# Kernel tuning notes

Measured on AMD Instinct MI355X. Metric: run time of the kernel, lower is better.

Reference implementation:

```python
import jax, jax.numpy as jnp
import numpy as np

N_NODES = 50000
N_EDGES = 800000
D_NODE = 128
D_EDGE = 64
N_GC = 2
H = 256
N_GRAPHS = 512


def setup_inputs() -> dict:
    key = jax.random.key(0)
    ks = jax.random.split(key, 32)
    s = 0.05
    inp = {
        'x': jax.random.normal(ks[0], (N_NODES, D_NODE), jnp.float32),
        'edge_index': jax.random.randint(ks[1], (2, N_EDGES), 0, N_NODES, jnp.int64 if jax.config.jax_enable_x64 else jnp.int32),
        'edge_attr': jax.random.normal(ks[2], (N_EDGES, D_EDGE), jnp.float32),
        'batch': jnp.sort(jax.random.randint(ks[3], (N_NODES,), 0, N_GRAPHS)),
    }
    zin = 2 * D_NODE + D_EDGE  # 320
    inp['conv_Wf'] = jax.random.normal(ks[4], (N_GC, D_NODE, zin), jnp.float32) * s
    inp['conv_bf'] = jnp.zeros((N_GC, D_NODE), jnp.float32)
    inp['conv_Ws'] = jax.random.normal(ks[5], (N_GC, D_NODE, zin), jnp.float32) * s
    inp['conv_bs'] = jnp.zeros((N_GC, D_NODE), jnp.float32)
    # mlp_1: Linear(128->256), ReLU, Linear(256->256), ReLU, proj Linear(256->128)
    inp['mlp1_W0'] = jax.random.normal(ks[6], (H, D_NODE), jnp.float32) * s
    inp['mlp1_b0'] = jnp.zeros((H,), jnp.float32)
    inp['mlp1_W1'] = jax.random.normal(ks[7], (H, H), jnp.float32) * s
    inp['mlp1_b1'] = jnp.zeros((H,), jnp.float32)
    inp['mlp1_Wp'] = jax.random.normal(ks[8], (D_NODE, H), jnp.float32) * s
    inp['mlp1_bp'] = jnp.zeros((D_NODE,), jnp.float32)
    # mlp_2: same structure
    inp['mlp2_W0'] = jax.random.normal(ks[9], (H, D_NODE), jnp.float32) * s
    inp['mlp2_b0'] = jnp.zeros((H,), jnp.float32)
    inp['mlp2_W1'] = jax.random.normal(ks[10], (H, H), jnp.float32) * s
    inp['mlp2_b1'] = jnp.zeros((H,), jnp.float32)
    inp['mlp2_Wp'] = jax.random.normal(ks[11], (D_NODE, H), jnp.float32) * s
    inp['mlp2_bp'] = jnp.zeros((D_NODE,), jnp.float32)
    inp['out_W'] = jax.random.normal(ks[12], (1, D_NODE), jnp.float32) * s
    inp['out_b'] = jnp.zeros((1,), jnp.float32)
    return inp


def _mlp(x, W0, b0, W1, b1, Wp, bp):
    h = jax.nn.relu(x @ W0.T + b0)
    h = jax.nn.relu(h @ W1.T + b1)
    return h @ Wp.T + bp


def _cgconv(x, src, dst, edge_attr, Wf, bf, Ws, bs):
    # z = [x_i (target), x_j (source), edge_attr]  -> [E, 2D+De]
    z = jnp.concatenate([x[dst], x[src], edge_attr], axis=-1)
    msg = jax.nn.sigmoid(z @ Wf.T + bf) * jax.nn.softplus(z @ Ws.T + bs)
    aggr = jax.ops.segment_sum(msg, dst, num_segments=x.shape[0])
    return x + aggr  # CGConv residual


def reference(x, edge_index, edge_attr, batch,
              conv_Wf, conv_bf, conv_Ws, conv_bs,
              mlp1_W0, mlp1_b0, mlp1_W1, mlp1_b1, mlp1_Wp, mlp1_bp,
              mlp2_W0, mlp2_b0, mlp2_W1, mlp2_b1, mlp2_Wp, mlp2_bp,
              out_W, out_b):
    src, dst = edge_index[0], edge_index[1]
    out = x
    for l in range(N_GC):
        out = _cgconv(out, src, dst, edge_attr, conv_Wf[l], conv_bf[l], conv_Ws[l], conv_bs[l])
    out = out + _mlp(out, mlp1_W0, mlp1_b0, mlp1_W1, mlp1_b1, mlp1_Wp, mlp1_bp)
    out = jax.ops.segment_sum(out, batch, num_segments=N_GRAPHS)  # global_add_pool
    out = out + _mlp(out, mlp2_W0, mlp2_b0, mlp2_W1, mlp2_b1, mlp2_Wp, mlp2_bp)
    out = out @ out_W.T + out_b  # [n_graphs, 1]
    return out
```

## Files before the change

### kernel.cpp

```cpp
#include <hip/hip_runtime.h>
#include <stdint.h>

#define NN 50000
#define NE 800000
#define DN 128
#define DE 64
#define NG 512
#define HD 256
#define LDA 72
#define SPK_S 132

typedef unsigned short ushort_t;
typedef __attribute__((ext_vector_type(8))) short short8;
typedef __attribute__((ext_vector_type(4))) float floatx4;

__device__ __forceinline__ float bf2f(ushort_t h){ unsigned u=((unsigned)h)<<16; float f; __builtin_memcpy(&f,&u,4); return f; }
__device__ __forceinline__ float bflo(unsigned u){ unsigned v=u<<16; float f; __builtin_memcpy(&f,&v,4); return f; }
__device__ __forceinline__ float bfhi(unsigned u){ unsigned v=u&0xffff0000u; float f; __builtin_memcpy(&f,&v,4); return f; }
__device__ __forceinline__ ushort_t f2bf(float f){ unsigned u; __builtin_memcpy(&u,&f,4); u += 0x7FFFu + ((u>>16)&1u); return (ushort_t)(u>>16); }
__device__ __forceinline__ unsigned pk2(float a,float b){ return (unsigned)f2bf(a) | ((unsigned)f2bf(b)<<16); }

__global__ void k_conv_node_w(const float* Wf, const float* Ws, ushort_t* out){
  int i = blockIdx.x*256 + threadIdx.x;
  if(i >= 2*512*128) return;
  int l = i >> 16;
  int r = i & 65535;
  int n = r >> 7, k = r & 127;
  const float* W = (n<256)? Wf : Ws;
  int nn = n & 127;
  int koff = ((n>>7)&1) ? 128+k : k;
  out[i] = f2bf(W[(size_t)l*128*320 + (size_t)nn*320 + koff]);
}

__global__ void k_conv_edge_w(const float* Wf, const float* Ws, ushort_t* out){
  int i = blockIdx.x*256 + threadIdx.x;
  if(i >= 2*256*64) return;
  int l = i >> 14;
  int r = i & 16383;
  int n = r >> 6, k = r & 63;
  const float* W = (n<128)? Wf : Ws;
  int nn = n & 127;
  out[i] = f2bf(W[(size_t)l*128*320 + (size_t)nn*320 + 256 + k]);
}

__global__ void k_f2bf(const float* s, ushort_t* d, int n){
  int i = blockIdx.x*256 + threadIdx.x;
  if(i<n) d[i] = f2bf(s[i]);
}

__global__ void k_init_x(const float* x, float* xcur, ushort_t* xb){
  int i = blockIdx.x*256 + threadIdx.x;
  if(i < NN*DN){ float v = x[i]; xcur[i]=v; xb[i]=f2bf(v); }
}

__global__ void k_zero_u32(unsigned* p, int n){
  int i = blockIdx.x*256 + threadIdx.x;
  if(i<n) p[i]=0u;
}

__global__ void k_hist(const int* dst, int* deg){
  int i = blockIdx.x*256 + threadIdx.x;
  if(i<NE) atomicAdd(&deg[dst[i]], 1);
}

__global__ void k_blocksum(const int* deg, int* bsum, int n){
  __shared__ int s[256];
  int t = threadIdx.x, i = blockIdx.x*256 + t;
  s[t] = (i<n)? deg[i] : 0;
  __syncthreads();
  for(int o=128;o>0;o>>=1){ if(t<o) s[t]+=s[t+o]; __syncthreads(); }
  if(t==0) bsum[blockIdx.x]=s[0];
}

__global__ void k_scan_bsum(int* bsum, int nb, int* offs, int nnodes){
  __shared__ int s[2][256];
  int t = threadIdx.x;
  int v = (t<nb)? bsum[t] : 0;
  s[0][t]=v; __syncthreads();
  int cur=0;
  for(int o=1;o<256;o<<=1){
    int nx=cur^1;
    s[nx][t] = s[cur][t] + ((t>=o)? s[cur][t-o] : 0);
    cur=nx; __syncthreads();
  }
  if(t<nb) bsum[t] = s[cur][t] - v;
  if(t==255) offs[nnodes] = s[cur][255];
}

__global__ void k_scanscatter(const int* deg, const int* bsum, int* offs, int* cursor, int n){
  __shared__ int s[2][256];
  int t=threadIdx.x, i=blockIdx.x*256+t;
  int v=(i<n)? deg[i] : 0;
  s[0][t]=v; __syncthreads();
  int cur=0;
  for(int o=1;o<256;o<<=1){
    int nx=cur^1;
    s[nx][t] = s[cur][t] + ((t>=o)? s[cur][t-o] : 0);
    cur=nx; __syncthreads();
  }
  if(i<n){ int ex = s[cur][t]-v + bsum[blockIdx.x]; offs[i]=ex; cursor[i]=ex; }
}

__global__ void k_scatter(const int* dst, int* cursor, int* eid){
  int i = blockIdx.x*256 + threadIdx.x;
  if(i<NE){ int pos = atomicAdd(&cursor[dst[i]], 1); eid[pos]=i; }
}

__global__ __launch_bounds__(256) void k_gemm(const ushort_t* __restrict__ Ain, const ushort_t* __restrict__ Wg,
      int M, int N, int K, const float* __restrict__ bias, int mode,
      ushort_t* __restrict__ outb, float* __restrict__ outf, const float* __restrict__ addf){
  __shared__ __align__(16) ushort_t As[64*LDA];
  __shared__ __align__(16) ushort_t Bs[64*LDA];
  int tid = threadIdx.x;
  int m0 = blockIdx.x*64, n0 = blockIdx.y*64;
  int w = tid>>6, lane = tid&63, row16 = lane&15, quad = lane>>4;
  floatx4 acc[4];
  #pragma unroll
  for(int t=0;t<4;t++) acc[t]=(floatx4)(0.f);
  int nk = K>>6;
  for(int kc=0; kc<nk; kc++){
    #pragma unroll
    for(int i=0;i<2;i++){
      int lin = tid + i*256;
      int row = lin>>3, c8 = (lin&7)*8;
      uint4 va;
      int gm = m0+row;
      if(gm < M) va = *(const uint4*)&Ain[(size_t)gm*K + kc*64 + c8];
      else va = make_uint4(0,0,0,0);
      *(uint4*)&As[row*LDA + c8] = va;
      uint4 vb = *(const uint4*)&Wg[(size_t)(n0+row)*K + kc*64 + c8];
      *(uint4*)&Bs[row*LDA + c8] = vb;
    }
    __syncthreads();
    #pragma unroll
    for(int ks=0;ks<2;ks++){
      short8 a = *(const short8*)&As[(w*16+row16)*LDA + ks*32 + quad*8];
      #pragma unroll
      for(int t=0;t<4;t++){
        short8 b = *(const short8*)&Bs[(t*16+row16)*LDA + ks*32 + quad*8];
        acc[t] = __builtin_amdgcn_mfma_f32_16x16x32_bf16(a,b,acc[t],0,0,0);
      }
    }
    __syncthreads();
  }
  #pragma unroll
  for(int t=0;t<4;t++){
    int nn = n0 + t*16 + row16;
    #pragma unroll
    for(int r=0;r<4;r++){
      int m = m0 + w*16 + quad*4 + r;
      if(m>=M) continue;
      float v = acc[t][r];
      if(mode==1){ v += bias[nn]; v = v>0.f? v:0.f; outb[(size_t)m*N+nn]=f2bf(v); }
      else if(mode==2){ v += bias[nn] + addf[(size_t)m*N+nn]; outf[(size_t)m*N+nn]=v; }
      else { outb[(size_t)m*N+nn]=f2bf(v); }
    }
  }
}

__global__ __launch_bounds__(256) void k_edge_msg(const float* __restrict__ ea,
      const int* __restrict__ src_g, const int* __restrict__ dst_g,
      const ushort_t* __restrict__ Wedge, const ushort_t* __restrict__ Atab,
      const float* __restrict__ bf, const float* __restrict__ bs,
      ushort_t* __restrict__ msg){
  __shared__ __align__(16) char smem[47616];
  ushort_t* We  = (ushort_t*)smem;
  unsigned* spk = (unsigned*)smem;
  ushort_t* el  = (ushort_t*)(smem + 36864);
  int*      dl  = (int*)(smem + 46080);
  int*      sl  = (int*)(smem + 46336);
  float*    bfl = (float*)(smem + 46592);
  float*    bsl = (float*)(smem + 47104);

  int tid = threadIdx.x;
  int e0 = blockIdx.x*64;
  {
    const uint4* s = (const uint4*)Wedge;
    #pragma unroll
    for(int i=0;i<8;i++){
      int idx = tid + i*256;
      int row = idx>>3, col = (idx&7)*8;
      *(uint4*)&We[row*LDA + col] = s[idx];
    }
  }
  {
    int row = tid>>2, c0 = (tid&3)*16;
    const float4* p = (const float4*)&ea[(size_t)(e0+row)*64 + c0];
    float4 f0=p[0], f1=p[1], f2=p[2], f3=p[3];
    uint4 q0, q1;
    q0.x=pk2(f0.x,f0.y); q0.y=pk2(f0.z,f0.w); q0.z=pk2(f1.x,f1.y); q0.w=pk2(f1.z,f1.w);
    q1.x=pk2(f2.x,f2.y); q1.y=pk2(f2.z,f2.w); q1.z=pk2(f3.x,f3.y); q1.w=pk2(f3.z,f3.w);
    *(uint4*)&el[row*LDA + c0] = q0;
    *(uint4*)&el[row*LDA + c0 + 8] = q1;
  }
  if(tid<64){ dl[tid]=dst_g[e0+tid]; sl[tid]=src_g[e0+tid]; }
  if(tid>=128 && tid<256){ int t2=tid-128; bfl[t2]=bf[t2]; }
  if(tid<128){ bsl[tid]=bs[tid]; }
  __syncthreads();

  int w = tid>>6, lane = tid&63, row16 = lane&15, quad = lane>>4;
  floatx4 acc[16];
  #pragma unroll
  for(int t=0;t<16;t++) acc[t]=(floatx4)(0.f);
  #pragma unroll
  for(int ks=0;ks<2;ks++){
    short8 a = *(const short8*)&el[(w*16+row16)*LDA + ks*32 + quad*8];
    #pragma unroll
    for(int t=0;t<16;t++){
      short8 b = *(const short8*)&We[(t*16+row16)*LDA + ks*32 + quad*8];
      acc[t]=__builtin_amdgcn_mfma_f32_16x16x32_bf16(a,b,acc[t],0,0,0);
    }
  }
  __syncthreads();

  #pragma unroll
  for(int t=0;t<8;t++){
    int c = t*16 + row16;
    float bfc = bfl[c], bsc = bsl[c];
    #pragma unroll
    for(int r=0;r<4;r++){
      int rl = w*16 + quad*4 + r;
      spk[rl*SPK_S + c] = pk2(acc[t][r] + bfc, acc[t+8][r] + bsc);
    }
  }
  __syncthreads();

  #pragma unroll
  for(int j=0;j<4;j++){
    int id  = j*256 + tid;
    int eli = id >> 4;
    int c0  = (id & 15) * 8;
    int d = dl[eli], s = sl[eli];
    const unsigned* base = &spk[eli*SPK_S + c0];
    uint4 q0 = *(const uint4*)(base);
    uint4 q1 = *(const uint4*)(base + 4);
    const ushort_t* Adp = Atab + (size_t)d*512;
    const ushort_t* Asp = Atab + (size_t)s*512;
    uint4 a0 = *(const uint4*)&Adp[c0];
    uint4 a1 = *(const uint4*)&Asp[128+c0];
    uint4 a2 = *(const uint4*)&Adp[256+c0];
    uint4 a3 = *(const uint4*)&Asp[384+c0];
    unsigned qs[8] = {q0.x,q0.y,q0.z,q0.w,q1.x,q1.y,q1.z,q1.w};
    unsigned A0[4] = {a0.x,a0.y,a0.z,a0.w};
    unsigned A1[4] = {a1.x,a1.y,a1.z,a1.w};
    unsigned A2[4] = {a2.x,a2.y,a2.z,a2.w};
    unsigned A3[4] = {a3.x,a3.y,a3.z,a3.w};
    unsigned outw[4];
    #pragma unroll
    for(int k=0;k<4;k++){
      float fv0 = bflo(qs[2*k])   + bflo(A0[k]) + bflo(A1[k]);
      float sv0 = bfhi(qs[2*k])   + bflo(A2[k]) + bflo(A3[k]);
      float fv1 = bflo(qs[2*k+1]) + bfhi(A0[k]) + bfhi(A1[k]);
      float sv1 = bfhi(qs[2*k+1]) + bfhi(A2[k]) + bfhi(A3[k]);
      float sig0 = 1.f/(1.f+__expf(-fv0));
      float sig1 = 1.f/(1.f+__expf(-fv1));
      float sp0  = fmaxf(sv0,0.f) + __logf(1.f+__expf(-fabsf(sv0)));
      float sp1  = fmaxf(sv1,0.f) + __logf(1.f+__expf(-fabsf(sv1)));
      outw[k] = pk2(sig0*sp0, sig1*sp1);
    }
    uint4 o4; o4.x=outw[0]; o4.y=outw[1]; o4.z=outw[2]; o4.w=outw[3];
    *(uint4*)&msg[(size_t)(e0+eli)*128 + c0] = o4;
  }
}

__global__ __launch_bounds__(256) void k_aggregate(const ushort_t* __restrict__ msg,
      const int* __restrict__ eid, const int* __restrict__ offs,
      float* __restrict__ xcur, ushort_t* __restrict__ xb){
  int v = blockIdx.x*4 + (threadIdx.x>>6);
  int lane = threadIdx.x & 63;
  int c0 = lane*2;
  float2 a = *(float2*)&xcur[(size_t)v*128 + c0];
  int b = offs[v], e_ = offs[v+1];
  for(int j=b;j<e_;j++){
    int e = eid[j];
    unsigned mm = *(const unsigned*)&msg[(size_t)e*128 + c0];
    a.x += bflo(mm);
    a.y += bfhi(mm);
  }
  *(float2*)&xcur[(size_t)v*128 + c0] = a;
  *(unsigned*)&xb[(size_t)v*128 + c0] = pk2(a.x, a.y);
}

__global__ __launch_bounds__(256) void k_pool(const float* __restrict__ xcur,
      const int* __restrict__ batch, float* __restrict__ pooled){
  int b0 = blockIdx.x * 128;
  int ch = threadIdx.x & 127;
  int half = threadIdx.x >> 7;
  int n0 = b0 + half*64;
  if(n0 >= NN) return;
  int n1 = n0 + 64; if(n1 > NN) n1 = NN;
  float sum = 0.f;
  int bid = batch[n0];
  for(int n=n0; n<n1; n++){
    int b = batch[n];
    if(b != bid){ atomicAdd(&pooled[(size_t)bid*128+ch], sum); sum=0.f; bid=b; }
    sum += xcur[(size_t)n*128 + ch];
  }
  atomicAdd(&pooled[(size_t)bid*128+ch], sum);
}

__global__ __launch_bounds__(256) void k_final(const float* __restrict__ pooled,
   const float* __restrict__ W0, const float* __restrict__ b0,
   const float* __restrict__ W1, const float* __restrict__ b1,
   const float* __restrict__ Wp, const float* __restrict__ bp,
   const float* __restrict__ outW, const float* __restrict__ outB,
   float* __restrict__ out){
  __shared__ float p[128], h0[256], h1[256], red[256];
  int g = blockIdx.x, t = threadIdx.x;
  if(t<128) p[t]=pooled[(size_t)g*128+t];
  __syncthreads();
  {
    const float4* wr = (const float4*)&W0[(size_t)t*128];
    float s=0.f;
    #pragma unroll 8
    for(int k=0;k<32;k++){ float4 wv=wr[k]; s += wv.x*p[k*4]+wv.y*p[k*4+1]+wv.z*p[k*4+2]+wv.w*p[k*4+3]; }
    s += b0[t]; h0[t] = s>0.f? s:0.f;
  }
  __syncthreads();
  {
    const float4* wr = (const float4*)&W1[(size_t)t*256];
    float s=0.f;
    #pragma unroll 8
    for(int k=0;k<64;k++){ float4 wv=wr[k]; s += wv.x*h0[k*4]+wv.y*h0[k*4+1]+wv.z*h0[k*4+2]+wv.w*h0[k*4+3]; }
    s += b1[t]; h1[t] = s>0.f? s:0.f;
  }
  __syncthreads();
  float rt = 0.f;
  if(t<128){
    const float4* wr=(const float4*)&Wp[(size_t)t*256];
    float s=0.f;
    #pragma unroll 8
    for(int k=0;k<64;k++){ float4 wv=wr[k]; s += wv.x*h1[k*4]+wv.y*h1[k*4+1]+wv.z*h1[k*4+2]+wv.w*h1[k*4+3]; }
    s += bp[t] + p[t];
    rt = s * outW[t];
  }
  red[t]=rt; __syncthreads();
  for(int o=128;o>0;o>>=1){ if(t<o) red[t]+=red[t+o]; __syncthreads(); }
  if(t==0) out[g] = red[0] + outB[0];
}

extern "C" void kernel_launch(void* const* d_in, const int* in_sizes, int n_in,
                              void* d_out, int out_size, void* d_ws, size_t ws_size,
                              hipStream_t stream){
  const float* x    = (const float*)d_in[0];
  const int*   ei   = (const int*)d_in[1];
  const float* ea   = (const float*)d_in[2];
  const int*   batch= (const int*)d_in[3];
  const float* cWf  = (const float*)d_in[4];
  const float* cbf  = (const float*)d_in[5];
  const float* cWs  = (const float*)d_in[6];
  const float* cbs  = (const float*)d_in[7];
  const float* W0   = (const float*)d_in[8];
  const float* b0   = (const float*)d_in[9];
  const float* W1   = (const float*)d_in[10];
  const float* b1   = (const float*)d_in[11];
  const float* Wp   = (const float*)d_in[12];
  const float* bp   = (const float*)d_in[13];
  const float* m2W0 = (const float*)d_in[14];
  const float* m2b0 = (const float*)d_in[15];
  const float* m2W1 = (const float*)d_in[16];
  const float* m2b1 = (const float*)d_in[17];
  const float* m2Wp = (const float*)d_in[18];
  const float* m2bp = (const float*)d_in[19];
  const float* outW = (const float*)d_in[20];
  const float* outB = (const float*)d_in[21];

  const int* srcp = ei;
  const int* dstp = ei + NE;

  char* ws = (char*)d_ws;
  size_t off = 0;
  auto alloc = [&](size_t bytes)->char*{
    char* p = ws + off;
    off += (bytes + 255) & ~(size_t)255;
    return p;
  };
  float*    xcur  = (float*)   alloc((size_t)NN*DN*4);
  ushort_t* xb    = (ushort_t*)alloc((size_t)NN*DN*2);
  ushort_t* Atab  = (ushort_t*)alloc((size_t)NN*512*2);
  ushort_t* msg   = (ushort_t*)alloc((size_t)NE*128*2);
  ushort_t* Wnode = (ushort_t*)alloc((size_t)2*512*128*2);
  ushort_t* Wedge = (ushort_t*)alloc((size_t)2*256*64*2);
  ushort_t* W0b   = (ushort_t*)alloc((size_t)256*128*2);
  ushort_t* W1b   = (ushort_t*)alloc((size_t)256*256*2);
  ushort_t* Wpb   = (ushort_t*)alloc((size_t)128*256*2);
  int*      deg   = (int*)     alloc((size_t)NN*4);
  int*      offs  = (int*)     alloc((size_t)(NN+1)*4);
  int*      cursor= (int*)     alloc((size_t)NN*4);
  int*      eid   = (int*)     alloc((size_t)NE*4);
  int*      bsum  = (int*)     alloc(256*4);
  float*    pooled= (float*)   alloc((size_t)NG*DN*4);
  ushort_t* h0 = Atab;
  ushort_t* h1 = Atab + (size_t)NN*256;

  k_conv_node_w<<<(2*512*128+255)/256, 256, 0, stream>>>(cWf, cWs, Wnode);
  k_conv_edge_w<<<(2*256*64+255)/256, 256, 0, stream>>>(cWf, cWs, Wedge);
  k_f2bf<<<(256*128+255)/256, 256, 0, stream>>>(W0, W0b, 256*128);
  k_f2bf<<<(256*256+255)/256, 256, 0, stream>>>(W1, W1b, 256*256);
  k_f2bf<<<(128*256+255)/256, 256, 0, stream>>>(Wp, Wpb, 128*256);
  k_init_x<<<(NN*DN+255)/256, 256, 0, stream>>>(x, xcur, xb);

  int nb = (NN+255)/256;
  k_zero_u32<<<(NN+255)/256, 256, 0, stream>>>((unsigned*)deg, NN);
  k_hist<<<(NE+255)/256, 256, 0, stream>>>(dstp, deg);
  k_blocksum<<<nb, 256, 0, stream>>>(deg, bsum, NN);
  k_scan_bsum<<<1, 256, 0, stream>>>(bsum, nb, offs, NN);
  k_scanscatter<<<nb, 256, 0, stream>>>(deg, bsum, offs, cursor, NN);
  k_scatter<<<(NE+255)/256, 256, 0, stream>>>(dstp, cursor, eid);

  for(int l=0;l<2;l++){
    dim3 ga((NN+63)/64, 512/64);
    k_gemm<<<ga, 256, 0, stream>>>(xb, Wnode + (size_t)l*512*128, NN, 512, 128,
                                   nullptr, 0, Atab, nullptr, nullptr);
    k_edge_msg<<<NE/64, 256, 0, stream>>>(ea, srcp, dstp, Wedge + (size_t)l*256*64,
                                          Atab, cbf + l*128, cbs + l*128, msg);
    k_aggregate<<<NN/4, 256, 0, stream>>>(msg, eid, offs, xcur, xb);
  }

  {
    dim3 g0((NN+63)/64, 256/64);
    k_gemm<<<g0, 256, 0, stream>>>(xb, W0b, NN, 256, 128, b0, 1, h0, nullptr, nullptr);
    dim3 g1((NN+63)/64, 256/64);
    k_gemm<<<g1, 256, 0, stream>>>(h0, W1b, NN, 256, 256, b1, 1, h1, nullptr, nullptr);
    dim3 g2((NN+63)/64, 128/64);
    k_gemm<<<g2, 256, 0, stream>>>(h1, Wpb, NN, 128, 256, bp, 2, nullptr, xcur, xcur);
  }

  k_zero_u32<<<(NG*DN+255)/256, 256, 0, stream>>>((unsigned*)pooled, NG*DN);
  k_pool<<<(NN+127)/128, 256, 0, stream>>>(xcur, batch, pooled);

  k_final<<<NG, 256, 0, stream>>>(pooled, m2W0, m2b0, m2W1, m2b1, m2Wp, m2bp,
                                  outW, outB, (float*)d_out);
  (void)in_sizes; (void)n_in; (void)out_size; (void)ws_size;
}
```

Baseline: 1.224 ms.

## Write edge messages in CSR order and vectorize aggregation, fuse weight prep

The edge message kernel now writes each message row straight to its destination-sorted CSR slot, so aggregation reads contiguous rows instead of gathering through an edge-id indirection. Aggregation uses 16-byte loads with four row slots per wavefront, combined by shuffles. The conv biases move into the node GEMM epilogue through a padded bias table. The activation uses hardware exp2/rcp/log intrinsics and a packed bf16 convert, and the five weight-conversion kernels are merged into one launch. In exchange, the message kernel's writes become scattered, and the approximate intrinsics may change numerics slightly.

Result: faster. 1.015 ms (-17.1%).

```diff
diff --git a/kernel.cpp b/kernel.cpp
--- a/kernel.cpp
+++ b/kernel.cpp
@@ -14,38 +14,61 @@
 typedef __attribute__((ext_vector_type(8))) short short8;
 typedef __attribute__((ext_vector_type(4))) float floatx4;
 
-__device__ __forceinline__ float bf2f(ushort_t h){ unsigned u=((unsigned)h)<<16; float f; __builtin_memcpy(&f,&u,4); return f; }
 __device__ __forceinline__ float bflo(unsigned u){ unsigned v=u<<16; float f; __builtin_memcpy(&f,&v,4); return f; }
 __device__ __forceinline__ float bfhi(unsigned u){ unsigned v=u&0xffff0000u; float f; __builtin_memcpy(&f,&v,4); return f; }
 __device__ __forceinline__ ushort_t f2bf(float f){ unsigned u; __builtin_memcpy(&u,&f,4); u += 0x7FFFu + ((u>>16)&1u); return (ushort_t)(u>>16); }
-__device__ __forceinline__ unsigned pk2(float a,float b){ return (unsigned)f2bf(a) | ((unsigned)f2bf(b)<<16); }
-
-__global__ void k_conv_node_w(const float* Wf, const float* Ws, ushort_t* out){
+__device__ __forceinline__ unsigned cvtpk(float a, float b){
+#if __has_builtin(__builtin_amdgcn_cvt_pk_bf16_f32)
+  auto r = __builtin_amdgcn_cvt_pk_bf16_f32(a,b);
+  unsigned u; __builtin_memcpy(&u,&r,4); return u;
+#else
+  return (unsigned)f2bf(a) | ((unsigned)f2bf(b)<<16);
+#endif
+}
+
+__device__ __forceinline__ float actv(float fv, float sv){
+  const float L2E = 1.44269504f, LN2 = 0.69314718f;
+  float ef  = __builtin_amdgcn_exp2f(-L2E*fv);
+  float sig = __builtin_amdgcn_rcpf(1.f+ef);
+  float t   = __builtin_amdgcn_exp2f(-L2E*fabsf(sv));
+  float sp  = fmaxf(sv,0.f) + LN2*__builtin_amdgcn_logf(1.f+t);
+  return sig*sp;
+}
+
+__global__ void k_prep(const float* __restrict__ Wf, const float* __restrict__ Ws,
+                       const float* __restrict__ W0, const float* __restrict__ W1, const float* __restrict__ Wp,
+                       const float* __restrict__ cbf, const float* __restrict__ cbs,
+                       ushort_t* Wnode, ushort_t* Wedge, ushort_t* W0b, ushort_t* W1b, ushort_t* Wpb,
+                       float* bias512){
   int i = blockIdx.x*256 + threadIdx.x;
-  if(i >= 2*512*128) return;
-  int l = i >> 16;
-  int r = i & 65535;
-  int n = r >> 7, k = r & 127;
-  const float* W = (n<256)? Wf : Ws;
-  int nn = n & 127;
-  int koff = ((n>>7)&1) ? 128+k : k;
-  out[i] = f2bf(W[(size_t)l*128*320 + (size_t)nn*320 + koff]);
-}
-
-__global__ void k_conv_edge_w(const float* Wf, const float* Ws, ushort_t* out){
-  int i = blockIdx.x*256 + threadIdx.x;
-  if(i >= 2*256*64) return;
-  int l = i >> 14;
-  int r = i & 16383;
-  int n = r >> 6, k = r & 63;
-  const float* W = (n<128)? Wf : Ws;
-  int nn = n & 127;
-  out[i] = f2bf(W[(size_t)l*128*320 + (size_t)nn*320 + 256 + k]);
-}
-
-__global__ void k_f2bf(const float* s, ushort_t* d, int n){
-  int i = blockIdx.x*256 + threadIdx.x;
-  if(i<n) d[i] = f2bf(s[i]);
+  if(i < 131072){
+    int l = i >> 16, r = i & 65535;
+    int n = r >> 7, k = r & 127;
+    const float* W = (n<256)? Wf : Ws;
+    int nn = n & 127;
+    int koff = ((n>>7)&1) ? 128+k : k;
+    Wnode[i] = f2bf(W[(size_t)l*128*320 + (size_t)nn*320 + koff]);
+  } else if(i < 163840){
+    int j = i - 131072;
+    int l = j >> 14, r = j & 16383;
+    int n = r >> 6, k = r & 63;
+    const float* W = (n<128)? Wf : Ws;
+    int nn = n & 127;
+    Wedge[j] = f2bf(W[(size_t)l*128*320 + (size_t)nn*320 + 256 + k]);
+  } else if(i < 196608){
+    int j = i - 163840; W0b[j] = f2bf(W0[j]);
+  } else if(i < 262144){
+    int j = i - 196608; W1b[j] = f2bf(W1[j]);
+  } else if(i < 294912){
+    int j = i - 262144; Wpb[j] = f2bf(Wp[j]);
+  } else if(i < 295936){
+    int j = i - 294912;
+    int l = j >> 9, c = j & 511;
+    float v = 0.f;
+    if(c < 128) v = cbf[l*128 + c];
+    else if(c >= 256 && c < 384) v = cbs[l*128 + (c-256)];
+    bias512[j] = v;
+  }
 }
 
 __global__ void k_init_x(const float* x, float* xcur, ushort_t* xb){
@@ -101,9 +124,9 @@
   if(i<n){ int ex = s[cur][t]-v + bsum[blockIdx.x]; offs[i]=ex; cursor[i]=ex; }
 }
 
-__global__ void k_scatter(const int* dst, int* cursor, int* eid){
+__global__ void k_scatter(const int* dst, int* cursor, int* csr_pos){
   int i = blockIdx.x*256 + threadIdx.x;
-  if(i<NE){ int pos = atomicAdd(&cursor[dst[i]], 1); eid[pos]=i; }
+  if(i<NE){ int pos = atomicAdd(&cursor[dst[i]], 1); csr_pos[i]=pos; }
 }
 
 __global__ __launch_bounds__(256) void k_gemm(const ushort_t* __restrict__ Ain, const ushort_t* __restrict__ Wg,
@@ -151,8 +174,9 @@
       int m = m0 + w*16 + quad*4 + r;
       if(m>=M) continue;
       float v = acc[t][r];
-      if(mode==1){ v += bias[nn]; v = v>0.f? v:0.f; outb[(size_t)m*N+nn]=f2bf(v); }
-      else if(mode==2){ v += bias[nn] + addf[(size_t)m*N+nn]; outf[(size_t)m*N+nn]=v; }
+      if(bias) v += bias[nn];
+      if(mode==1){ v = v>0.f? v:0.f; outb[(size_t)m*N+nn]=f2bf(v); }
+      else if(mode==2){ v += addf[(size_t)m*N+nn]; outf[(size_t)m*N+nn]=v; }
       else { outb[(size_t)m*N+nn]=f2bf(v); }
     }
   }
@@ -160,17 +184,16 @@
 
 __global__ __launch_bounds__(256) void k_edge_msg(const float* __restrict__ ea,
       const int* __restrict__ src_g, const int* __restrict__ dst_g,
+      const int* __restrict__ csr_pos,
       const ushort_t* __restrict__ Wedge, const ushort_t* __restrict__ Atab,
-      const float* __restrict__ bf, const float* __restrict__ bs,
       ushort_t* __restrict__ msg){
-  __shared__ __align__(16) char smem[47616];
+  __shared__ __align__(16) char smem[46848];
   ushort_t* We  = (ushort_t*)smem;
   unsigned* spk = (unsigned*)smem;
   ushort_t* el  = (ushort_t*)(smem + 36864);
   int*      dl  = (int*)(smem + 46080);
   int*      sl  = (int*)(smem + 46336);
-  float*    bfl = (float*)(smem + 46592);
-  float*    bsl = (float*)(smem + 47104);
+  int*      cp  = (int*)(smem + 46592);
 
   int tid = threadIdx.x;
   int e0 = blockIdx.x*64;
@@ -188,14 +211,13 @@
     const float4* p = (const float4*)&ea[(size_t)(e0+row)*64 + c0];
     float4 f0=p[0], f1=p[1], f2=p[2], f3=p[3];
     uint4 q0, q1;
-    q0.x=pk2(f0.x,f0.y); q0.y=pk2(f0.z,f0.w); q0.z=pk2(f1.x,f1.y); q0.w=pk2(f1.z,f1.w);
-    q1.x=pk2(f2.x,f2.y); q1.y=pk2(f2.z,f2.w); q1.z=pk2(f3.x,f3.y); q1.w=pk2(f3.z,f3.w);
+    q0.x=cvtpk(f0.x,f0.y); q0.y=cvtpk(f0.z,f0.w); q0.z=cvtpk(f1.x,f1.y); q0.w=cvtpk(f1.z,f1.w);
+    q1.x=cvtpk(f2.x,f2.y); q1.y=cvtpk(f2.z,f2.w); q1.z=cvtpk(f3.x,f3.y); q1.w=cvtpk(f3.z,f3.w);
     *(uint4*)&el[row*LDA + c0] = q0;
     *(uint4*)&el[row*LDA + c0 + 8] = q1;
   }
   if(tid<64){ dl[tid]=dst_g[e0+tid]; sl[tid]=src_g[e0+tid]; }
-  if(tid>=128 && tid<256){ int t2=tid-128; bfl[t2]=bf[t2]; }
-  if(tid<128){ bsl[tid]=bs[tid]; }
+  else if(tid>=64 && tid<128){ cp[tid-64]=csr_pos[e0+tid-64]; }
   __syncthreads();
 
   int w = tid>>6, lane = tid&63, row16 = lane&15, quad = lane>>4;
@@ -216,11 +238,10 @@
   #pragma unroll
   for(int t=0;t<8;t++){
     int c = t*16 + row16;
-    float bfc = bfl[c], bsc = bsl[c];
     #pragma unroll
     for(int r=0;r<4;r++){
       int rl = w*16 + quad*4 + r;
-      spk[rl*SPK_S + c] = pk2(acc[t][r] + bfc, acc[t+8][r] + bsc);
+      spk[rl*SPK_S + c] = cvtpk(acc[t][r], acc[t+8][r]);
     }
   }
   __syncthreads();
@@ -230,7 +251,7 @@
     int id  = j*256 + tid;
     int eli = id >> 4;
     int c0  = (id & 15) * 8;
-    int d = dl[eli], s = sl[eli];
+    int d = dl[eli], s = sl[eli], mrow = cp[eli];
     const unsigned* base = &spk[eli*SPK_S + c0];
     uint4 q0 = *(const uint4*)(base);
     uint4 q1 = *(const uint4*)(base + 4);
@@ -252,33 +273,45 @@
       float sv0 = bfhi(qs[2*k])   + bflo(A2[k]) + bflo(A3[k]);
       float fv1 = bflo(qs[2*k+1]) + bfhi(A0[k]) + bfhi(A1[k]);
       float sv1 = bfhi(qs[2*k+1]) + bfhi(A2[k]) + bfhi(A3[k]);
-      float sig0 = 1.f/(1.f+__expf(-fv0));
-      float sig1 = 1.f/(1.f+__expf(-fv1));
-      float sp0  = fmaxf(sv0,0.f) + __logf(1.f+__expf(-fabsf(sv0)));
-      float sp1  = fmaxf(sv1,0.f) + __logf(1.f+__expf(-fabsf(sv1)));
-      outw[k] = pk2(sig0*sp0, sig1*sp1);
+      outw[k] = cvtpk(actv(fv0,sv0), actv(fv1,sv1));
     }
     uint4 o4; o4.x=outw[0]; o4.y=outw[1]; o4.z=outw[2]; o4.w=outw[3];
-    *(uint4*)&msg[(size_t)(e0+eli)*128 + c0] = o4;
+    *(uint4*)&msg[(size_t)mrow*128 + c0] = o4;
   }
 }
 
 __global__ __launch_bounds__(256) void k_aggregate(const ushort_t* __restrict__ msg,
-      const int* __restrict__ eid, const int* __restrict__ offs,
-      float* __restrict__ xcur, ushort_t* __restrict__ xb){
+      const int* __restrict__ offs, float* __restrict__ xcur, ushort_t* __restrict__ xb){
   int v = blockIdx.x*4 + (threadIdx.x>>6);
   int lane = threadIdx.x & 63;
-  int c0 = lane*2;
-  float2 a = *(float2*)&xcur[(size_t)v*128 + c0];
-  int b = offs[v], e_ = offs[v+1];
-  for(int j=b;j<e_;j++){
-    int e = eid[j];
-    unsigned mm = *(const unsigned*)&msg[(size_t)e*128 + c0];
-    a.x += bflo(mm);
-    a.y += bfhi(mm);
-  }
-  *(float2*)&xcur[(size_t)v*128 + c0] = a;
-  *(unsigned*)&xb[(size_t)v*128 + c0] = pk2(a.x, a.y);
+  int rslot = lane>>4;
+  int c0 = (lane&15)*8;
+  int b = offs[v], e = offs[v+1];
+  float acc[8];
+  #pragma unroll
+  for(int k=0;k<8;k++) acc[k]=0.f;
+  for(int r=b+rslot; r<e; r+=4){
+    uint4 m = *(const uint4*)&msg[(size_t)r*128 + c0];
+    acc[0]+=bflo(m.x); acc[1]+=bfhi(m.x);
+    acc[2]+=bflo(m.y); acc[3]+=bfhi(m.y);
+    acc[4]+=bflo(m.z); acc[5]+=bfhi(m.z);
+    acc[6]+=bflo(m.w); acc[7]+=bfhi(m.w);
+  }
+  #pragma unroll
+  for(int k=0;k<8;k++){
+    acc[k] += __shfl_xor(acc[k],16);
+    acc[k] += __shfl_xor(acc[k],32);
+  }
+  if(rslot==0){
+    float4 x0 = *(float4*)&xcur[(size_t)v*128+c0];
+    float4 x1 = *(float4*)&xcur[(size_t)v*128+c0+4];
+    x0.x+=acc[0]; x0.y+=acc[1]; x0.z+=acc[2]; x0.w+=acc[3];
+    x1.x+=acc[4]; x1.y+=acc[5]; x1.z+=acc[6]; x1.w+=acc[7];
+    *(float4*)&xcur[(size_t)v*128+c0]=x0;
+    *(float4*)&xcur[(size_t)v*128+c0+4]=x1;
+    uint4 o; o.x=cvtpk(x0.x,x0.y); o.y=cvtpk(x0.z,x0.w); o.z=cvtpk(x1.x,x1.y); o.w=cvtpk(x1.z,x1.w);
+    *(uint4*)&xb[(size_t)v*128+c0]=o;
+  }
 }
 
 __global__ __launch_bounds__(256) void k_pool(const float* __restrict__ xcur,
@@ -375,29 +408,27 @@
     off += (bytes + 255) & ~(size_t)255;
     return p;
   };
-  float*    xcur  = (float*)   alloc((size_t)NN*DN*4);
-  ushort_t* xb    = (ushort_t*)alloc((size_t)NN*DN*2);
-  ushort_t* Atab  = (ushort_t*)alloc((size_t)NN*512*2);
-  ushort_t* msg   = (ushort_t*)alloc((size_t)NE*128*2);
-  ushort_t* Wnode = (ushort_t*)alloc((size_t)2*512*128*2);
-  ushort_t* Wedge = (ushort_t*)alloc((size_t)2*256*64*2);
-  ushort_t* W0b   = (ushort_t*)alloc((size_t)256*128*2);
-  ushort_t* W1b   = (ushort_t*)alloc((size_t)256*256*2);
-  ushort_t* Wpb   = (ushort_t*)alloc((size_t)128*256*2);
-  int*      deg   = (int*)     alloc((size_t)NN*4);
-  int*      offs  = (int*)     alloc((size_t)(NN+1)*4);
-  int*      cursor= (int*)     alloc((size_t)NN*4);
-  int*      eid   = (int*)     alloc((size_t)NE*4);
-  int*      bsum  = (int*)     alloc(256*4);
-  float*    pooled= (float*)   alloc((size_t)NG*DN*4);
+  float*    xcur   = (float*)   alloc((size_t)NN*DN*4);
+  ushort_t* xb     = (ushort_t*)alloc((size_t)NN*DN*2);
+  ushort_t* Atab   = (ushort_t*)alloc((size_t)NN*512*2);
+  ushort_t* msg    = (ushort_t*)alloc((size_t)NE*128*2);
+  ushort_t* Wnode  = (ushort_t*)alloc((size_t)2*512*128*2);
+  ushort_t* Wedge  = (ushort_t*)alloc((size_t)2*256*64*2);
+  ushort_t* W0b    = (ushort_t*)alloc((size_t)256*128*2);
+  ushort_t* W1b    = (ushort_t*)alloc((size_t)256*256*2);
+  ushort_t* Wpb    = (ushort_t*)alloc((size_t)128*256*2);
+  float*    bias512= (float*)   alloc((size_t)2*512*4);
+  int*      deg    = (int*)     alloc((size_t)NN*4);
+  int*      offs   = (int*)     alloc((size_t)(NN+1)*4);
+  int*      cursor = (int*)     alloc((size_t)NN*4);
+  int*      csr_pos= (int*)     alloc((size_t)NE*4);
+  int*      bsum   = (int*)     alloc(256*4);
+  float*    pooled = (float*)   alloc((size_t)NG*DN*4);
   ushort_t* h0 = Atab;
   ushort_t* h1 = Atab + (size_t)NN*256;
 
-  k_conv_node_w<<<(2*512*128+255)/256, 256, 0, stream>>>(cWf, cWs, Wnode);
-  k_conv_edge_w<<<(2*256*64+255)/256, 256, 0, stream>>>(cWf, cWs, Wedge);
-  k_f2bf<<<(256*128+255)/256, 256, 0, stream>>>(W0, W0b, 256*128);
-  k_f2bf<<<(256*256+255)/256, 256, 0, stream>>>(W1, W1b, 256*256);
-  k_f2bf<<<(128*256+255)/256, 256, 0, stream>>>(Wp, Wpb, 128*256);
+  k_prep<<<1156, 256, 0, stream>>>(cWf, cWs, W0, W1, Wp, cbf, cbs,
+                                   Wnode, Wedge, W0b, W1b, Wpb, bias512);
   k_init_x<<<(NN*DN+255)/256, 256, 0, stream>>>(x, xcur, xb);
 
   int nb = (NN+255)/256;
@@ -406,15 +437,15 @@
   k_blocksum<<<nb, 256, 0, stream>>>(deg, bsum, NN);
   k_scan_bsum<<<1, 256, 0, stream>>>(bsum, nb, offs, NN);
   k_scanscatter<<<nb, 256, 0, stream>>>(deg, bsum, offs, cursor, NN);
-  k_scatter<<<(NE+255)/256, 256, 0, stream>>>(dstp, cursor, eid);
+  k_scatter<<<(NE+255)/256, 256, 0, stream>>>(dstp, cursor, csr_pos);
 
   for(int l=0;l<2;l++){
     dim3 ga((NN+63)/64, 512/64);
     k_gemm<<<ga, 256, 0, stream>>>(xb, Wnode + (size_t)l*512*128, NN, 512, 128,
-                                   nullptr, 0, Atab, nullptr, nullptr);
-    k_edge_msg<<<NE/64, 256, 0, stream>>>(ea, srcp, dstp, Wedge + (size_t)l*256*64,
-                                          Atab, cbf + l*128, cbs + l*128, msg);
-    k_aggregate<<<NN/4, 256, 0, stream>>>(msg, eid, offs, xcur, xb);
+                                   bias512 + l*512, 0, Atab, nullptr, nullptr);
+    k_edge_msg<<<NE/64, 256, 0, stream>>>(ea, srcp, dstp, csr_pos,
+                                          Wedge + (size_t)l*256*64, Atab, msg);
+    k_aggregate<<<NN/4, 256, 0, stream>>>(msg, offs, xcur, xb);
   }
 
   {
```
